# Performance work log

Hardware: AMD Instinct MI355X
Metric: run time of the kernel (lower is better)

## Reference

```python
import jax, jax.numpy as jnp
import numpy as np

# dims
IMG = 24; B = 2; C = 3; N = IMG * IMG + 1        # 577 tokens (patch size 1 + cls)
DIM = 512; DEPTH = 2; H = 8; DH = 64; MLP = 2048; NCLS = 1000
SW = 32      # sliding window size
CB = 16      # compress block size
CS = 4       # compress block sliding stride
SB = 64      # selection block size
KSEL = 4     # num selected blocks


def _ln(x, g, b):
    m = x.mean(-1, keepdims=True)
    v = ((x - m) ** 2).mean(-1, keepdims=True)
    return (x - m) * jax.lax.rsqrt(v + 1e-5) * g + b


# gather rows per (batch, head): t [n, d], i [n, m] -> [n, m, d]
_gather = jax.vmap(jax.vmap(lambda t, i: t[i]))


def _sparse_attn(x, Wq, Wk, Wv, Wg, Wo, kpe, vpe, Wkc, Wvc):
    """Native-sparse-attention (non-causal): compress + top-k block select + sliding window,
    combined with per-head sigmoid gates computed from the input."""
    b, n, _ = x.shape
    split = lambda t: t.reshape(b, n, H, DH).transpose(0, 2, 1, 3)   # [b,h,n,dh]
    q = split(x @ Wq); k = split(x @ Wk); v = split(x @ Wv)
    scale = DH ** -0.5

    # ---- compressed branch: overlapping blocks of size CB, stride CS, MLP-compressed ----
    nc = -(-n // CS)
    pad = (nc - 1) * CS + CB - n
    kp = jnp.pad(k, ((0, 0), (0, 0), (0, pad), (0, 0)))
    vp = jnp.pad(v, ((0, 0), (0, 0), (0, pad), (0, 0)))
    widx = jnp.arange(nc)[:, None] * CS + jnp.arange(CB)[None, :]    # [nc, CB]
    kw = kp[:, :, widx] + kpe                                        # [b,h,nc,CB,dh]
    vw = vp[:, :, widx] + vpe
    ck = kw.reshape(b, H, nc, CB * DH) @ Wkc                         # [b,h,nc,dh]
    cv = vw.reshape(b, H, nc, CB * DH) @ Wvc
    sc = jnp.einsum('bhid,bhjd->bhij', q, ck) * scale                # [b,h,n,nc]
    pc = jax.nn.softmax(sc, axis=-1)
    out_c = jnp.einsum('bhij,bhjd->bhid', pc, cv)

    # ---- selection branch: map compressed-block scores to selection blocks, top-k ----
    ns = -(-n // SB)
    centers = jnp.clip((jnp.arange(nc) * CS + CB // 2) // SB, 0, ns - 1)
    M = jax.nn.one_hot(centers, ns, dtype=pc.dtype)                  # [nc, ns]
    imp = jnp.einsum('bhij,js->bhis', pc, M)                         # [b,h,n,ns]
    _, selb = jax.lax.top_k(imp, KSEL)                               # [b,h,n,KSEL]
    tok = (selb[..., None] * SB + jnp.arange(SB)).reshape(b, H, n, KSEL * SB)
    mask = tok < n
    tokc = jnp.minimum(tok, n - 1)
    kg = _gather(k, tokc)                                            # [b,h,n,KSEL*SB,dh]
    vg = _gather(v, tokc)
    ss = jnp.einsum('bhid,bhikd->bhik', q, kg) * scale
    ss = jnp.where(mask, ss, -jnp.inf)
    ps = jax.nn.softmax(ss, axis=-1)
    out_s = jnp.einsum('bhik,bhikd->bhid', ps, vg)

    # ---- sliding window branch ----
    off = jnp.arange(SW) - SW // 2
    pos = jnp.arange(n)[:, None] + off                               # [n, SW]
    wmask = (pos >= 0) & (pos < n)
    posc = jnp.clip(pos, 0, n - 1)
    kwn = k[:, :, posc]; vwn = v[:, :, posc]                         # [b,h,n,SW,dh]
    sw = jnp.einsum('bhid,bhiwd->bhiw', q, kwn) * scale
    sw = jnp.where(wmask, sw, -jnp.inf)
    pw = jax.nn.softmax(sw, axis=-1)
    out_w = jnp.einsum('bhiw,bhiwd->bhid', pw, vwn)

    # ---- gated combine ----
    g = jax.nn.sigmoid(x @ Wg).reshape(b, n, H, 3).transpose(0, 2, 1, 3)  # [b,h,n,3]
    out = g[..., 0:1] * out_c + g[..., 1:2] * out_s + g[..., 2:3] * out_w
    return out.transpose(0, 2, 1, 3).reshape(b, n, H * DH) @ Wo


def _forward(img, patch_w, patch_b, pos_emb, cls_tok, ln1_g, ln1_b, Wq, Wk, Wv,
             Wg, Wo, kpe, vpe, Wkc, Wvc, ln2_g, ln2_b, ff_w1, ff_b1, ff_w2,
             ff_b2, hln_g, hln_b, head_w, head_b):
    b = img.shape[0]
    # patch size 1: b c h w -> b (h w) c, then linear embed
    x = img.transpose(0, 2, 3, 1).reshape(b, IMG * IMG, C) @ patch_w + patch_b
    x = jnp.concatenate([jnp.broadcast_to(cls_tok, (b, 1, DIM)), x], axis=1)
    x = x + pos_emb[:, :x.shape[1]]
    for l in range(DEPTH):
        h = _ln(x, ln1_g[l], ln1_b[l])
        x = _sparse_attn(h, Wq[l], Wk[l], Wv[l], Wg[l], Wo[l], kpe[l], vpe[l], Wkc[l], Wvc[l]) + x
        h = _ln(x, ln2_g[l], ln2_b[l])
        x = (jax.nn.gelu(h @ ff_w1[l] + ff_b1[l]) @ ff_w2[l] + ff_b2[l]) + x
    x = _ln(x[:, 0], hln_g, hln_b)   # cls pool + head LayerNorm
    return x @ head_w + head_b


def setup_inputs() -> dict:
    key = jax.random.key(0)
    ks = jax.random.split(key, 20)
    rn = lambda k, shape, s=0.02: jax.random.normal(k, shape, dtype=jnp.float32) * s
    d = {}
    d['img'] = jax.random.normal(ks[0], (B, C, IMG, IMG), dtype=jnp.float32)
    d['patch_w'] = rn(ks[1], (C, DIM), 0.2)
    d['patch_b'] = jnp.zeros((DIM,), jnp.float32)
    d['pos_emb'] = rn(ks[2], (1, N, DIM))
    d['cls_tok'] = rn(ks[3], (1, 1, DIM))
    d['ln1_g'] = jnp.ones((DEPTH, DIM), jnp.float32)
    d['ln1_b'] = jnp.zeros((DEPTH, DIM), jnp.float32)
    d['Wq'] = rn(ks[4], (DEPTH, DIM, H * DH))
    d['Wk'] = rn(ks[5], (DEPTH, DIM, H * DH))
    d['Wv'] = rn(ks[6], (DEPTH, DIM, H * DH))
    d['Wg'] = rn(ks[7], (DEPTH, DIM, 3 * H))
    d['Wo'] = rn(ks[8], (DEPTH, H * DH, DIM))
    d['kpe'] = rn(ks[9], (DEPTH, CB, DH))
    d['vpe'] = rn(ks[10], (DEPTH, CB, DH))
    d['Wkc'] = rn(ks[11], (DEPTH, CB * DH, DH))
    d['Wvc'] = rn(ks[12], (DEPTH, CB * DH, DH))
    d['ln2_g'] = jnp.ones((DEPTH, DIM), jnp.float32)
    d['ln2_b'] = jnp.zeros((DEPTH, DIM), jnp.float32)
    d['ff_w1'] = rn(ks[13], (DEPTH, DIM, MLP))
    d['ff_b1'] = jnp.zeros((DEPTH, MLP), jnp.float32)
    d['ff_w2'] = rn(ks[14], (DEPTH, MLP, DIM))
    d['ff_b2'] = jnp.zeros((DEPTH, DIM), jnp.float32)
    d['hln_g'] = jnp.ones((DIM,), jnp.float32)
    d['hln_b'] = jnp.zeros((DIM,), jnp.float32)
    d['head_w'] = rn(ks[15], (DIM, NCLS))
    d['head_b'] = jnp.zeros((NCLS,), jnp.float32)
    return d


def reference(img, patch_w, patch_b, pos_emb, cls_tok, ln1_g, ln1_b, Wq, Wk, Wv,
              Wg, Wo, kpe, vpe, Wkc, Wvc, ln2_g, ln2_b, ff_w1, ff_b1, ff_w2,
              ff_b2, hln_g, hln_b, head_w, head_b):
    return _forward(img, patch_w, patch_b, pos_emb, cls_tok, ln1_g, ln1_b, Wq, Wk, Wv,
                    Wg, Wo, kpe, vpe, Wkc, Wvc, ln2_g, ln2_b, ff_w1, ff_b1, ff_w2,
                    ff_b2, hln_g, hln_b, head_w, head_b)
```

## Files before the change

### kernel.cpp

```cpp
#include <hip/hip_runtime.h>
#include <math.h>


#define NTOK 577
#define DIMD 512
#define NH 8
#define DHD 64
#define NC 145
#define NSB 10
#define KSELD 4
#define SBD 64
#define CBD 16
#define CSD 4
#define SWD 32
#define MLPD 2048
#define NCLSD 1000
#define BATCH 2
#define QKVN 1536
#define QKVNG 1600
#define SFSTRIDE 592
#define SCSTRIDE 160
#define PSTRIDE 832
#define MCKD 2320

typedef unsigned short ushort;
typedef __attribute__((ext_vector_type(8))) short short8;
typedef __attribute__((ext_vector_type(4))) short short4v;
typedef __attribute__((ext_vector_type(4))) float f32x4;

#if defined(__has_builtin)
#if __has_builtin(__builtin_amdgcn_global_load_lds)
#define HAVE_GLL 1
#endif
#endif

#ifdef HAVE_GLL
__device__ __forceinline__ void gll16(const ushort* g, short* l) {
  __builtin_amdgcn_global_load_lds(
      (const __attribute__((address_space(1))) unsigned int*)g,
      (__attribute__((address_space(3))) unsigned int*)l, 16, 0, 0);
}
#endif

__device__ __forceinline__ ushort bf16_rne(float f) {
  union { float f; unsigned u; } v; v.f = f;
  unsigned u = v.u;
  unsigned r = (u + 0x7fffu + ((u >> 16) & 1u)) >> 16;
  return (ushort)r;
}
__device__ __forceinline__ float bf16_to_f(ushort s) {
  union { unsigned u; float f; } v; v.u = ((unsigned)s) << 16;
  return v.f;
}
__device__ __forceinline__ int imin(int a, int b) { return a < b ? a : b; }
__device__ __forceinline__ int imax(int a, int b) { return a > b ? a : b; }

__global__ void prep_kernel(const float* __restrict__ Wq, const float* __restrict__ Wk,
                            const float* __restrict__ Wv, const float* __restrict__ Wg,
                            const float* __restrict__ Wo, const float* __restrict__ Wkc,
                            const float* __restrict__ Wvc, const float* __restrict__ w1,
                            const float* __restrict__ w2,
                            ushort* __restrict__ wqkv_t, ushort* __restrict__ wo_t,
                            ushort* __restrict__ w1_t, ushort* __restrict__ w2_t,
                            ushort* __restrict__ wkc_t, ushort* __restrict__ wvc_t,
                            const float* __restrict__ img, const float* __restrict__ pw,
                            const float* __restrict__ pb, const float* __restrict__ pos,
                            const float* __restrict__ cls, float* __restrict__ x) {
  int bid = blockIdx.x;
  int tid = threadIdx.x;
  if (bid >= 6464) {
    int idx = (bid - 6464) * 256 + tid;
    const int total = BATCH * NTOK * DIMD;
    if (idx >= total) return;
    int d = idx & (DIMD - 1);
    int i = (idx / DIMD) % NTOK;
    int b = idx / (DIMD * NTOK);
    float val;
    if (i == 0) {
      val = cls[d];
    } else {
      int p = i - 1;
      val = pb[d];
#pragma unroll
      for (int c = 0; c < 3; ++c)
        val += img[b * 3 * 576 + c * 576 + p] * pw[c * DIMD + d];
    }
    x[idx] = val + pos[i * DIMD + d];
    return;
  }
  __shared__ float tile[32][33];
  int l = bid / 3232;
  int t = bid % 3232;
  const float* W; ushort* Wt; int K, N, bx, by;
  if (t < 768) {
    int which = t >> 8, rr = t & 255;
    W = (which == 0 ? Wq : (which == 1 ? Wk : Wv)) + (long)l * 512 * 512;
    Wt = wqkv_t + (long)l * QKVNG * 512 + which * 512 * 512;
    K = 512; N = 512; bx = rr & 15; by = rr >> 4;
  } else if (t < 1024) {
    int rr = t - 768; W = Wo + (long)l * 512 * 512; Wt = wo_t + (long)l * 512 * 512;
    K = 512; N = 512; bx = rr & 15; by = rr >> 4;
  } else if (t < 2048) {
    int rr = t - 1024; W = w1 + (long)l * 512 * 2048; Wt = w1_t + (long)l * 2048 * 512;
    K = 512; N = 2048; bx = rr & 63; by = rr >> 6;
  } else if (t < 3072) {
    int rr = t - 2048; W = w2 + (long)l * 2048 * 512; Wt = w2_t + (long)l * 512 * 2048;
    K = 2048; N = 512; bx = rr & 15; by = rr >> 4;
  } else if (t < 3104) {
    int rr = t - 3072; W = Wg + (long)l * 512 * 24;
    Wt = wqkv_t + (long)l * QKVNG * 512 + (long)1536 * 512;
    K = 512; N = 24; bx = rr & 1; by = rr >> 1;
  } else if (t < 3168) {
    int rr = t - 3104; W = Wkc + (long)l * 1024 * 64; Wt = wkc_t + (long)l * 64 * 1024;
    K = 1024; N = 64; bx = rr & 1; by = rr >> 1;
  } else {
    int rr = t - 3168; W = Wvc + (long)l * 1024 * 64; Wt = wvc_t + (long)l * 64 * 1024;
    K = 1024; N = 64; bx = rr & 1; by = rr >> 1;
  }
  int k0 = by * 32, n0 = bx * 32;
  int tx = tid & 31, ty = tid >> 5;
#pragma unroll
  for (int r = 0; r < 32; r += 8)
    tile[ty + r][tx] = (n0 + tx < N) ? W[(long)(k0 + ty + r) * N + n0 + tx] : 0.f;
  __syncthreads();
#pragma unroll
  for (int r = 0; r < 32; r += 8)
    Wt[(long)(n0 + ty + r) * K + k0 + tx] = bf16_rne(tile[tx][ty + r]);
}

__global__ void ln_kernel(const float* __restrict__ x, const float* __restrict__ g,
                          const float* __restrict__ bb, ushort* __restrict__ out_bf) {
  int row = blockIdx.x;
  const float* xr = x + (long)row * DIMD;
  int t = threadIdx.x;
  float a = xr[t], c = xr[t + 256];
  __shared__ float s1[256], s2[256];
  s1[t] = a + c;
  s2[t] = a * a + c * c;
  __syncthreads();
  for (int off = 128; off > 0; off >>= 1) {
    if (t < off) { s1[t] += s1[t + off]; s2[t] += s2[t + off]; }
    __syncthreads();
  }
  float m = s1[0] * (1.0f / 512.0f);
  float var = s2[0] * (1.0f / 512.0f) - m * m;
  float r = rsqrtf(var + 1e-5f);
  out_bf[(long)row * DIMD + t] = bf16_rne((a - m) * r * g[t] + bb[t]);
  out_bf[(long)row * DIMD + t + 256] = bf16_rne((c - m) * r * g[t + 256] + bb[t + 256]);
}

__global__ __launch_bounds__(256) void mfma_gemm(
    const ushort* __restrict__ A, const ushort* __restrict__ Bt,
    const float* __restrict__ bias,
    float* __restrict__ Cf, ushort* __restrict__ Cbf, float* __restrict__ gb,
    int M, int N, int K, int kSlice, int mode) {
  int tid = threadIdx.x;
  int lane = tid & 63, wave = tid >> 6;
  int wm = wave >> 1, wn = wave & 1;
  int rowBase = blockIdx.y * 64, colBase = blockIdx.x * 64;
  int m = lane & 15, kg = lane >> 4;
  int kBeg = blockIdx.z * kSlice;
  int kEnd = imin(K, kBeg + kSlice);
  f32x4 acc[2][2] = {};
#ifdef HAVE_GLL
  __shared__ short As[64 * 64];
  __shared__ short Bs[64 * 64];
  int r8 = lane >> 3;
  int cs = (lane & 7) ^ r8;
  const ushort* aG0 = A + (long)(rowBase + wave * 8 + r8) * K + cs * 8 + kBeg;
  const ushort* aG1 = aG0 + (long)32 * K;
  const ushort* bG0 = Bt + (long)(colBase + wave * 8 + r8) * K + cs * 8 + kBeg;
  const ushort* bG1 = bG0 + (long)32 * K;
  short* lA0 = &As[(wave * 8) * 64];
  short* lA1 = &As[(wave * 8 + 32) * 64];
  short* lB0 = &Bs[(wave * 8) * 64];
  short* lB1 = &Bs[(wave * 8 + 32) * 64];
  int xa = m & 7;
  for (int k0 = 0; k0 < kEnd - kBeg; k0 += 64) {
    gll16(aG0 + k0, lA0);
    gll16(aG1 + k0, lA1);
    gll16(bG0 + k0, lB0);
    gll16(bG1 + k0, lB1);
    __syncthreads();
#pragma unroll
    for (int ks = 0; ks < 2; ++ks) {
      int kc = ks * 4 + kg;
      short8 a0 = *(const short8*)&As[(wm * 32 + m) * 64 + (kc ^ xa) * 8];
      short8 a1 = *(const short8*)&As[(wm * 32 + 16 + m) * 64 + (kc ^ xa) * 8];
      short8 b0 = *(const short8*)&Bs[(wn * 32 + m) * 64 + (kc ^ xa) * 8];
      short8 b1 = *(const short8*)&Bs[(wn * 32 + 16 + m) * 64 + (kc ^ xa) * 8];
      acc[0][0] = __builtin_amdgcn_mfma_f32_16x16x32_bf16(a0, b0, acc[0][0], 0, 0, 0);
      acc[0][1] = __builtin_amdgcn_mfma_f32_16x16x32_bf16(a0, b1, acc[0][1], 0, 0, 0);
      acc[1][0] = __builtin_amdgcn_mfma_f32_16x16x32_bf16(a1, b0, acc[1][0], 0, 0, 0);
      acc[1][1] = __builtin_amdgcn_mfma_f32_16x16x32_bf16(a1, b1, acc[1][1], 0, 0, 0);
    }
    __syncthreads();
  }
#else
  __shared__ short As[64][72];
  __shared__ short Bs[64][72];
  for (int k0 = kBeg; k0 < kEnd; k0 += 64) {
#pragma unroll
    for (int cc = 0; cc < 2; ++cc) {
      int c = tid * 2 + cc;
      int r = c >> 3, kc = c & 7;
      short8 av = {};
      int gr = rowBase + r;
      if (gr < M) av = *(const short8*)(A + (long)gr * K + k0 + kc * 8);
      *(short8*)&As[r][kc * 8] = av;
      short8 bv = *(const short8*)(Bt + (long)(colBase + r) * K + k0 + kc * 8);
      *(short8*)&Bs[r][kc * 8] = bv;
    }
    __syncthreads();
#pragma unroll
    for (int ks = 0; ks < 2; ++ks) {
      short8 a0 = *(const short8*)&As[wm * 32 + m][ks * 32 + kg * 8];
      short8 a1 = *(const short8*)&As[wm * 32 + 16 + m][ks * 32 + kg * 8];
      short8 b0 = *(const short8*)&Bs[wn * 32 + m][ks * 32 + kg * 8];
      short8 b1 = *(const short8*)&Bs[wn * 32 + 16 + m][ks * 32 + kg * 8];
      acc[0][0] = __builtin_amdgcn_mfma_f32_16x16x32_bf16(a0, b0, acc[0][0], 0, 0, 0);
      acc[0][1] = __builtin_amdgcn_mfma_f32_16x16x32_bf16(a0, b1, acc[0][1], 0, 0, 0);
      acc[1][0] = __builtin_amdgcn_mfma_f32_16x16x32_bf16(a1, b0, acc[1][0], 0, 0, 0);
      acc[1][1] = __builtin_amdgcn_mfma_f32_16x16x32_bf16(a1, b1, acc[1][1], 0, 0, 0);
    }
    __syncthreads();
  }
#endif
#pragma unroll
  for (int mt = 0; mt < 2; ++mt)
#pragma unroll
    for (int nt = 0; nt < 2; ++nt) {
      int col = colBase + wn * 32 + nt * 16 + m;
#pragma unroll
      for (int r = 0; r < 4; ++r) {
        int row = rowBase + wm * 32 + mt * 16 + kg * 4 + r;
        if (row >= M) continue;
        float v = acc[mt][nt][r];
        if (mode == 2) {
          if (col < QKVN) Cbf[(long)row * QKVN + col] = bf16_rne(v);
          else if (col < QKVNG) gb[(long)row * 64 + (col - QKVN)] = 1.f / (1.f + __expf(-v));
        } else if (mode == 1) {
          v += bias[col];
          float u = 0.7978845608028654f * (v + 0.044715f * v * v * v);
          v = 0.5f * v * (1.f + tanhf(u));
          Cbf[(long)row * N + col] = bf16_rne(v);
        } else {
          if (bias && blockIdx.z == 0) v += bias[col];
          atomicAdd(&Cf[(long)row * N + col], v);
        }
      }
    }
}

__global__ __launch_bounds__(256) void ckcv_gemm(
    const ushort* __restrict__ kwm, const ushort* __restrict__ vwm,
    const ushort* __restrict__ wkc_t, const ushort* __restrict__ wvc_t,
    ushort* __restrict__ ckb, ushort* __restrict__ Vt) {
  const int K = 1024;
  bool cvpath = blockIdx.z != 0;
  const ushort* A  = cvpath ? wvc_t : kwm;
  const ushort* Bt = cvpath ? vwm : wkc_t;
  int rowBase = cvpath ? 0 : blockIdx.y * 64;
  int colBase = cvpath ? blockIdx.y * 64 : 0;
  int aRows = cvpath ? 64 : MCKD;
  int bRows = cvpath ? MCKD : 64;
  __shared__ short As[64][72];
  __shared__ short Bs[64][72];
  int tid = threadIdx.x;
  int lane = tid & 63, wave = tid >> 6;
  int wm = wave >> 1, wn = wave & 1;
  int m = lane & 15, kg = lane >> 4;
  f32x4 acc[2][2] = {};
  for (int k0 = 0; k0 < K; k0 += 64) {
#pragma unroll
    for (int cc = 0; cc < 2; ++cc) {
      int c = tid * 2 + cc;
      int r = c >> 3, kc = c & 7;
      short8 av = {};
      if (rowBase + r < aRows) av = *(const short8*)(A + (long)(rowBase + r) * K + k0 + kc * 8);
      *(short8*)&As[r][kc * 8] = av;
      short8 bv = {};
      if (colBase + r < bRows) bv = *(const short8*)(Bt + (long)(colBase + r) * K + k0 + kc * 8);
      *(short8*)&Bs[r][kc * 8] = bv;
    }
    __syncthreads();
#pragma unroll
    for (int ks = 0; ks < 2; ++ks) {
      short8 a0 = *(const short8*)&As[wm * 32 + m][ks * 32 + kg * 8];
      short8 a1 = *(const short8*)&As[wm * 32 + 16 + m][ks * 32 + kg * 8];
      short8 b0 = *(const short8*)&Bs[wn * 32 + m][ks * 32 + kg * 8];
      short8 b1 = *(const short8*)&Bs[wn * 32 + 16 + m][ks * 32 + kg * 8];
      acc[0][0] = __builtin_amdgcn_mfma_f32_16x16x32_bf16(a0, b0, acc[0][0], 0, 0, 0);
      acc[0][1] = __builtin_amdgcn_mfma_f32_16x16x32_bf16(a0, b1, acc[0][1], 0, 0, 0);
      acc[1][0] = __builtin_amdgcn_mfma_f32_16x16x32_bf16(a1, b0, acc[1][0], 0, 0, 0);
      acc[1][1] = __builtin_amdgcn_mfma_f32_16x16x32_bf16(a1, b1, acc[1][1], 0, 0, 0);
    }
    __syncthreads();
  }
#pragma unroll
  for (int mt = 0; mt < 2; ++mt)
#pragma unroll
    for (int nt = 0; nt < 2; ++nt) {
      int col = colBase + wn * 32 + nt * 16 + m;
#pragma unroll
      for (int r = 0; r < 4; ++r) {
        int row = rowBase + wm * 32 + mt * 16 + kg * 4 + r;
        float v = acc[mt][nt][r];
        if (!cvpath) {
          if (row < MCKD) ckb[(long)row * DHD + col] = bf16_rne(v);
        } else {
          if (col < MCKD) {
            int z16 = col / NC, j = col - z16 * NC;
            Vt[((long)z16 * 64 + row) * PSTRIDE + 640 + j] = bf16_rne(v);
          }
        }
      }
    }
}

__global__ __launch_bounds__(256) void score_kernel(
    const ushort* __restrict__ qkv_bf, const ushort* __restrict__ ckb,
    ushort* __restrict__ Sf, ushort* __restrict__ Scb, float scale) {
  __shared__ short As[64][72];
  __shared__ short Bs[64][72];
  int z = blockIdx.z;
  int b = z >> 3, h = z & 7;
  int i0 = blockIdx.y * 64;
  int xb = blockIdx.x;
  bool isC = xb >= 10;
  int j0 = (isC ? (xb - 10) : xb) * 64;
  int tid = threadIdx.x;
  int lane = tid & 63, wave = tid >> 6;
  int wm = wave >> 1, wn = wave & 1;
  const ushort* aBase = qkv_bf + (long)b * NTOK * QKVN + h * 64;
  const ushort* bBase = aBase + 512;
  const ushort* cBase = ckb + (long)z * NC * DHD;
#pragma unroll
  for (int rep = 0; rep < 4; ++rep) {
    int row = rep * 16 + (tid >> 4);
    int c4 = tid & 15;
    int gi = i0 + row;
    short4v a16 = {};
    if (gi < NTOK) a16 = *(const short4v*)(aBase + (long)gi * QKVN + c4 * 4);
    *(short4v*)&As[row][c4 * 4] = a16;
    int gj = j0 + row;
    short4v b16 = {};
    if (isC) {
      if (gj < NC) b16 = *(const short4v*)(cBase + (long)gj * DHD + c4 * 4);
    } else {
      if (gj < NTOK) b16 = *(const short4v*)(bBase + (long)gj * QKVN + c4 * 4);
    }
    *(short4v*)&Bs[row][c4 * 4] = b16;
  }
  __syncthreads();
  int m = lane & 15, kg = lane >> 4;
  f32x4 acc[2][2] = {};
#pragma unroll
  for (int ks = 0; ks < 2; ++ks) {
    short8 a0 = *(const short8*)&As[wm * 32 + m][ks * 32 + kg * 8];
    short8 a1 = *(const short8*)&As[wm * 32 + 16 + m][ks * 32 + kg * 8];
    short8 b0 = *(const short8*)&Bs[wn * 32 + m][ks * 32 + kg * 8];
    short8 b1 = *(const short8*)&Bs[wn * 32 + 16 + m][ks * 32 + kg * 8];
    acc[0][0] = __builtin_amdgcn_mfma_f32_16x16x32_bf16(a0, b0, acc[0][0], 0, 0, 0);
    acc[0][1] = __builtin_amdgcn_mfma_f32_16x16x32_bf16(a0, b1, acc[0][1], 0, 0, 0);
    acc[1][0] = __builtin_amdgcn_mfma_f32_16x16x32_bf16(a1, b0, acc[1][0], 0, 0, 0);
    acc[1][1] = __builtin_amdgcn_mfma_f32_16x16x32_bf16(a1, b1, acc[1][1], 0, 0, 0);
  }
  int nvalid = isC ? NC : NTOK;
  int sstride = isC ? SCSTRIDE : SFSTRIDE;
  ushort* Sz = (isC ? Scb : Sf) + (long)z * NTOK * sstride;
#pragma unroll
  for (int mt = 0; mt < 2; ++mt)
#pragma unroll
    for (int nt = 0; nt < 2; ++nt) {
      int col = j0 + wn * 32 + nt * 16 + m;
#pragma unroll
      for (int r = 0; r < 4; ++r) {
        int row = i0 + wm * 32 + mt * 16 + kg * 4 + r;
        if (row < NTOK && col < nvalid)
          Sz[(long)row * sstride + col] = bf16_rne(acc[mt][nt][r] * scale);
      }
    }
}

__global__ void kwvt_kernel(const ushort* __restrict__ qkv_bf,
                            const float* __restrict__ kpe, const float* __restrict__ vpe,
                            ushort* __restrict__ kwm, ushort* __restrict__ vwm,
                            ushort* __restrict__ Vt) {
  __shared__ short tile[64][72];
  int bid = blockIdx.x;
  if (bid < MCKD) {
    int j = bid % NC;
    int bh = bid / NC;
    int h = bh & 7, b = bh >> 3;
    int t = threadIdx.x >> 4;
    int d4 = threadIdx.x & 15;
    int tok = j * CSD + t;
    float k0 = 0.f, k1 = 0.f, k2 = 0.f, k3 = 0.f, v0 = 0.f, v1 = 0.f, v2 = 0.f, v3 = 0.f;
    if (tok < NTOK) {
      const ushort* base = qkv_bf + (long)(b * NTOK + tok) * QKVN + h * DHD + d4 * 4;
      short4v kv = *(const short4v*)(base + 512);
      short4v vv = *(const short4v*)(base + 1024);
      k0 = bf16_to_f((ushort)kv.x); k1 = bf16_to_f((ushort)kv.y);
      k2 = bf16_to_f((ushort)kv.z); k3 = bf16_to_f((ushort)kv.w);
      v0 = bf16_to_f((ushort)vv.x); v1 = bf16_to_f((ushort)vv.y);
      v2 = bf16_to_f((ushort)vv.z); v3 = bf16_to_f((ushort)vv.w);
    }
    float4 kp = *(const float4*)(kpe + t * DHD + d4 * 4);
    float4 vp = *(const float4*)(vpe + t * DHD + d4 * 4);
    short4v ko, vo;
    ko.x = (short)bf16_rne(k0 + kp.x); ko.y = (short)bf16_rne(k1 + kp.y);
    ko.z = (short)bf16_rne(k2 + kp.z); ko.w = (short)bf16_rne(k3 + kp.w);
    vo.x = (short)bf16_rne(v0 + vp.x); vo.y = (short)bf16_rne(v1 + vp.y);
    vo.z = (short)bf16_rne(v2 + vp.z); vo.w = (short)bf16_rne(v3 + vp.w);
    long ob = (long)bid * 1024 + t * DHD + d4 * 4;
    *(short4v*)(kwm + ob) = ko;
    *(short4v*)(vwm + ob) = vo;
  } else {
    int t = bid - MCKD;
    int kt = t % 10, z = t / 10;
    int b = z >> 3, h = z & 7;
    int tid = threadIdx.x;
    int r = tid >> 2, seg = tid & 3;
    short8 a0 = {}, a1 = {};
    int tok = kt * 64 + r;
    if (tok < NTOK) {
      const ushort* src = qkv_bf + (long)(b * NTOK + tok) * QKVN + 1024 + h * 64 + seg * 16;
      a0 = *(const short8*)src;
      a1 = *(const short8*)(src + 8);
    }
    *(short8*)&tile[r][seg * 16] = a0;
    *(short8*)&tile[r][seg * 16 + 8] = a1;
    __syncthreads();
    int d = tid >> 2;
    short8 o0, o1;
#pragma unroll
    for (int q = 0; q < 8; ++q) o0[q] = tile[seg * 16 + q][d];
#pragma unroll
    for (int q = 0; q < 8; ++q) o1[q] = tile[seg * 16 + 8 + q][d];
    ushort* dst = Vt + ((long)z * 64 + d) * PSTRIDE + kt * 64 + seg * 16;
    *(short8*)dst = o0;
    *(short8*)(dst + 8) = o1;
  }
}

__global__ __launch_bounds__(256, 4) void prob_kernel(
    const ushort* __restrict__ Sf, const ushort* __restrict__ Scb,
    const float* __restrict__ gb, ushort* __restrict__ P) {
  int qt = blockIdx.x % NC;
  int z = blockIdx.x / NC;
  int h = z & 7, b = z >> 3;
  int tid = threadIdx.x, lane = tid & 63, w = tid >> 6;
  int i0 = qt * 4 + w;
  bool valid = i0 < NTOK;
  int i = imin(i0, NTOK - 1);

  __shared__ float scL[4][192];
  __shared__ float ssL[4][256];
  __shared__ float swL[4][32];
  __shared__ float impL[4][16];
  __shared__ int selL[4][KSELD];
  float* sc = scL[w]; float* ss = ssL[w];
  float* swv = swL[w]; float* imp = impL[w]; int* sel = selL[w];

  const ushort* scRow = Scb + ((long)z * NTOK + i) * SCSTRIDE;
  const ushort* sfRow = Sf + ((long)z * NTOK + i) * SFSTRIDE;

  float e[3], mC = -1e30f;
#pragma unroll
  for (int c = 0; c < 3; ++c) {
    int j = c * 64 + lane;
    float s = bf16_to_f(scRow[imin(j, NC - 1)]);
    s = (j < NC) ? s : -1e30f;
    e[c] = s;
    mC = fmaxf(mC, s);
  }
#pragma unroll
  for (int msk = 1; msk < 64; msk <<= 1) mC = fmaxf(mC, __shfl_xor(mC, msk, 64));
  float sumC = 0.f;
#pragma unroll
  for (int c = 0; c < 3; ++c) {
    float ev = (e[c] > -1e29f) ? __expf(e[c] - mC) : 0.f;
    sc[c * 64 + lane] = ev;
    sumC += ev;
  }
#pragma unroll
  for (int msk = 1; msk < 64; msk <<= 1) sumC += __shfl_xor(sumC, msk, 64);
  __syncthreads();

  if (lane < NSB) {
    int lo = imax(0, 16 * lane - 2), hi = imin(NC - 1, 16 * lane + 13);
    float s = 0.f;
    for (int j = lo; j <= hi; ++j) s += sc[j];
    imp[lane] = s;
  }
  __syncthreads();
  if (lane == 0) {
    unsigned used = 0;
    for (int r = 0; r < KSELD; ++r) {
      int bi = 0; float bv = -1e30f;
      for (int s = 0; s < NSB; ++s)
        if (!((used >> s) & 1u) && imp[s] > bv) { bv = imp[s]; bi = s; }
      used |= 1u << bi;
      sel[r] = bi;
    }
  }
  __syncthreads();

  float es[4], mS = -1e30f;
#pragma unroll
  for (int c = 0; c < 4; ++c) {
    int tok = sel[c] * SBD + lane;
    float s = bf16_to_f(sfRow[imin(tok, NTOK - 1)]);
    s = (tok < NTOK) ? s : -1e30f;
    es[c] = s;
    mS = fmaxf(mS, s);
  }
#pragma unroll
  for (int msk = 1; msk < 64; msk <<= 1) mS = fmaxf(mS, __shfl_xor(mS, msk, 64));
  float sumS = 0.f;
#pragma unroll
  for (int c = 0; c < 4; ++c) {
    float ev = (es[c] > -1e29f) ? __expf(es[c] - mS) : 0.f;
    ss[c * 64 + lane] = ev;
    sumS += ev;
  }
#pragma unroll
  for (int msk = 1; msk < 64; msk <<= 1) sumS += __shfl_xor(sumS, msk, 64);

  float sw_s;
  {
    int pos = i + (lane & 31) - SWD / 2;
    float s = bf16_to_f(sfRow[imin(imax(pos, 0), NTOK - 1)]);
    sw_s = (pos >= 0 && pos < NTOK) ? s : -1e30f;
  }
  float mW = sw_s;
#pragma unroll
  for (int msk = 1; msk < 32; msk <<= 1) mW = fmaxf(mW, __shfl_xor(mW, msk, 64));
  float ew = (sw_s > -1e29f) ? __expf(sw_s - mW) : 0.f;
  float sumW = ew;
#pragma unroll
  for (int msk = 1; msk < 32; msk <<= 1) sumW += __shfl_xor(sumW, msk, 64);
  if (lane < SWD) swv[lane] = ew;
  __syncthreads();

  if (!valid) return;
  const float* gp = gb + (long)(b * NTOK + i) * 64 + h * 3;
  float rC = gp[0] / sumC, rS = gp[1] / sumS, rW = gp[2] / sumW;
  ushort* prow = P + ((long)z * NTOK + i0) * PSTRIDE;
#pragma unroll
  for (int c = 0; c < 10; ++c) {
    int col = c * 64 + lane;
    float val = 0.f;
#pragma unroll
    for (int r = 0; r < 4; ++r)
      if (sel[r] == c) val += rS * ss[r * 64 + lane];
    int t = col - i + 16;
    if (t >= 0 && t < SWD && col < NTOK) val += rW * swv[t];
    prow[col] = bf16_rne(val);
  }
#pragma unroll
  for (int c = 0; c < 3; ++c) {
    int j = c * 64 + lane;
    float val = (j < NC) ? rC * sc[j] : 0.f;
    prow[640 + j] = bf16_rne(val);
  }
}

__global__ __launch_bounds__(256) void pv_gemm(const ushort* __restrict__ P,
                                               const ushort* __restrict__ Vt,
                                               ushort* __restrict__ comb) {
  __shared__ short As[64][72];
  __shared__ short Bs[64][72];
  int z = blockIdx.y;
  int b = z >> 3, h = z & 7;
  int rowBase = blockIdx.x * 64;
  int tid = threadIdx.x;
  int lane = tid & 63, wave = tid >> 6;
  int wm = wave >> 1, wn = wave & 1;
  const ushort* Pz = P + (long)z * NTOK * PSTRIDE;
  const ushort* Vz = Vt + (long)z * 64 * PSTRIDE;
  int m = lane & 15, kg = lane >> 4;
  f32x4 acc[2][2] = {};
  for (int k0 = 0; k0 < PSTRIDE; k0 += 64) {
#pragma unroll
    for (int cc = 0; cc < 2; ++cc) {
      int c = tid * 2 + cc;
      int r = c >> 3, kc = c & 7;
      short8 av = {};
      int gr = rowBase + r;
      if (gr < NTOK) av = *(const short8*)(Pz + (long)gr * PSTRIDE + k0 + kc * 8);
      *(short8*)&As[r][kc * 8] = av;
      short8 bv = *(const short8*)(Vz + (long)r * PSTRIDE + k0 + kc * 8);
      *(short8*)&Bs[r][kc * 8] = bv;
    }
    __syncthreads();
#pragma unroll
    for (int ks = 0; ks < 2; ++ks) {
      short8 a0 = *(const short8*)&As[wm * 32 + m][ks * 32 + kg * 8];
      short8 a1 = *(const short8*)&As[wm * 32 + 16 + m][ks * 32 + kg * 8];
      short8 b0 = *(const short8*)&Bs[wn * 32 + m][ks * 32 + kg * 8];
      short8 b1 = *(const short8*)&Bs[wn * 32 + 16 + m][ks * 32 + kg * 8];
      acc[0][0] = __builtin_amdgcn_mfma_f32_16x16x32_bf16(a0, b0, acc[0][0], 0, 0, 0);
      acc[0][1] = __builtin_amdgcn_mfma_f32_16x16x32_bf16(a0, b1, acc[0][1], 0, 0, 0);
      acc[1][0] = __builtin_amdgcn_mfma_f32_16x16x32_bf16(a1, b0, acc[1][0], 0, 0, 0);
      acc[1][1] = __builtin_amdgcn_mfma_f32_16x16x32_bf16(a1, b1, acc[1][1], 0, 0, 0);
    }
    __syncthreads();
  }
#pragma unroll
  for (int mt = 0; mt < 2; ++mt)
#pragma unroll
    for (int nt = 0; nt < 2; ++nt) {
      int col = wn * 32 + nt * 16 + m;
#pragma unroll
      for (int r = 0; r < 4; ++r) {
        int row = rowBase + wm * 32 + mt * 16 + kg * 4 + r;
        if (row < NTOK)
          comb[(long)(b * NTOK + row) * DIMD + h * 64 + col] = bf16_rne(acc[mt][nt][r]);
      }
    }
}

__global__ void head_kernel(const float* __restrict__ x, const float* __restrict__ hg,
                            const float* __restrict__ hb, const float* __restrict__ W,
                            const float* __restrict__ bias, float* __restrict__ out) {
  int b = blockIdx.y;
  int tid = threadIdx.x;
  const float* xr = x + (long)b * NTOK * DIMD;
  __shared__ float red1[256], red2[256];
  float a = xr[tid], c = xr[tid + 256];
  red1[tid] = a + c;
  red2[tid] = a * a + c * c;
  __syncthreads();
  for (int off = 128; off > 0; off >>= 1) {
    if (tid < off) { red1[tid] += red1[tid + off]; red2[tid] += red2[tid + off]; }
    __syncthreads();
  }
  float m = red1[0] * (1.f / 512.f);
  float var = red2[0] * (1.f / 512.f) - m * m;
  float rs = rsqrtf(var + 1e-5f);
  __shared__ float hs[512];
  hs[tid] = (a - m) * rs * hg[tid] + hb[tid];
  hs[tid + 256] = (c - m) * rs * hg[tid + 256] + hb[tid + 256];
  __syncthreads();
  int col = blockIdx.x * 64 + (tid & 63);
  int ks = tid >> 6;
  float acc = 0.f;
  if (col < NCLSD) {
    for (int k = ks * 128; k < ks * 128 + 128; ++k)
      acc += hs[k] * W[(long)k * NCLSD + col];
  }
  __shared__ float part[4][64];
  part[ks][tid & 63] = acc;
  __syncthreads();
  if (tid < 64) {
    int c2 = blockIdx.x * 64 + tid;
    if (c2 < NCLSD)
      out[b * NCLSD + c2] = part[0][tid] + part[1][tid] + part[2][tid] + part[3][tid] + bias[c2];
  }
}

extern "C" void kernel_launch(void* const* d_in, const int* in_sizes, int n_in,
                              void* d_out, int out_size, void* d_ws, size_t ws_size,
                              hipStream_t stream) {
  const float* img     = (const float*)d_in[0];
  const float* patch_w = (const float*)d_in[1];
  const float* patch_b = (const float*)d_in[2];
  const float* pos_emb = (const float*)d_in[3];
  const float* cls_tok = (const float*)d_in[4];
  const float* ln1_g   = (const float*)d_in[5];
  const float* ln1_b   = (const float*)d_in[6];
  const float* Wq      = (const float*)d_in[7];
  const float* Wk      = (const float*)d_in[8];
  const float* Wv      = (const float*)d_in[9];
  const float* Wg      = (const float*)d_in[10];
  const float* Wo      = (const float*)d_in[11];
  const float* kpe     = (const float*)d_in[12];
  const float* vpe     = (const float*)d_in[13];
  const float* Wkc     = (const float*)d_in[14];
  const float* Wvc     = (const float*)d_in[15];
  const float* ln2_g   = (const float*)d_in[16];
  const float* ln2_b   = (const float*)d_in[17];
  const float* ff_w1   = (const float*)d_in[18];
  const float* ff_b1   = (const float*)d_in[19];
  const float* ff_w2   = (const float*)d_in[20];
  const float* ff_b2   = (const float*)d_in[21];
  const float* hln_g   = (const float*)d_in[22];
  const float* hln_b   = (const float*)d_in[23];
  const float* head_w  = (const float*)d_in[24];
  const float* head_b  = (const float*)d_in[25];
  float* out = (float*)d_out;

  char* p = (char*)d_ws;
  const long MROW = (long)BATCH * NTOK;
  float* x       = (float*)p;  p += MROW * DIMD * 4;
  ushort* qkv_bf = (ushort*)p; p += MROW * QKVN * 2;
  ushort* h_bf   = (ushort*)p; p += MROW * DIMD * 2;
  ushort* comb_bf= (ushort*)p; p += MROW * DIMD * 2;
  float* gb      = (float*)p;  p += MROW * 64 * 4;
  ushort* ckb    = (ushort*)p; p += (long)MCKD * DHD * 2;
  ushort* Vt     = (ushort*)p; p += (long)BATCH * NH * 64 * PSTRIDE * 2;
  ushort* Scb    = (ushort*)p; p += (long)BATCH * NH * NTOK * SCSTRIDE * 2;
  ushort* wqkv_t = (ushort*)p; p += 2L * QKVNG * DIMD * 2;
  ushort* wo_t   = (ushort*)p; p += 2L * DIMD * DIMD * 2;
  ushort* w1_t   = (ushort*)p; p += 2L * MLPD * DIMD * 2;
  ushort* w2_t   = (ushort*)p; p += 2L * DIMD * MLPD * 2;
  ushort* wkc_t  = (ushort*)p; p += 2L * 64 * 1024 * 2;
  ushort* wvc_t  = (ushort*)p; p += 2L * 64 * 1024 * 2;
  ushort* kwm    = (ushort*)p;
  ushort* vwm    = kwm + (long)MCKD * 1024;
  ushort* P      = kwm;
  p += (long)BATCH * NH * NTOK * PSTRIDE * 2;
  ushort* Sf     = (ushort*)p;
  ushort* ff1_bf = Sf;
  p += (long)BATCH * NH * NTOK * SFSTRIDE * 2;
  p += 64 * 2048 * 2;

  const int M = (int)MROW;
  const int MB64 = (M + 63) / 64;
  const float scale = 0.125f;

  prep_kernel<<<6464 + (int)((M * DIMD + 255) / 256), 256, 0, stream>>>(
      Wq, Wk, Wv, Wg, Wo, Wkc, Wvc, ff_w1, ff_w2,
      wqkv_t, wo_t, w1_t, w2_t, wkc_t, wvc_t,
      img, patch_w, patch_b, pos_emb, cls_tok, x);

  for (int l = 0; l < 2; ++l) {
    const ushort* wqkv_l = wqkv_t + (long)l * QKVNG * DIMD;
    const ushort* wo_l   = wo_t + (long)l * DIMD * DIMD;
    const ushort* w1t_l  = w1_t + (long)l * MLPD * DIMD;
    const ushort* w2t_l  = w2_t + (long)l * DIMD * MLPD;
    const ushort* wkc_l  = wkc_t + (long)l * 64 * 1024;
    const ushort* wvc_l  = wvc_t + (long)l * 64 * 1024;
    const float* kpe_l = kpe + (long)l * CBD * DHD;
    const float* vpe_l = vpe + (long)l * CBD * DHD;
    const float* b1_l  = ff_b1 + (long)l * MLPD;
    const float* b2_l  = ff_b2 + (long)l * DIMD;

    ln_kernel<<<M, 256, 0, stream>>>(x, ln1_g + (long)l * DIMD, ln1_b + (long)l * DIMD, h_bf);
    mfma_gemm<<<dim3(QKVNG / 64, MB64), 256, 0, stream>>>(h_bf, wqkv_l, nullptr, nullptr, qkv_bf, gb, M, QKVNG, DIMD, DIMD, 2);
    kwvt_kernel<<<MCKD + 160, 256, 0, stream>>>(qkv_bf, kpe_l, vpe_l, kwm, vwm, Vt);
    ckcv_gemm<<<dim3(1, (MCKD + 63) / 64, 2), 256, 0, stream>>>(kwm, vwm, wkc_l, wvc_l, ckb, Vt);
    score_kernel<<<dim3(13, 10, BATCH * NH), 256, 0, stream>>>(qkv_bf, ckb, Sf, Scb, scale);
    prob_kernel<<<BATCH * NH * NC, 256, 0, stream>>>(Sf, Scb, gb, P);
    pv_gemm<<<dim3(10, BATCH * NH), 256, 0, stream>>>(P, Vt, comb_bf);
    mfma_gemm<<<dim3(DIMD / 64, MB64, 2), 256, 0, stream>>>(comb_bf, wo_l, nullptr, x, nullptr, nullptr, M, DIMD, DIMD, 256, 4);
    ln_kernel<<<M, 256, 0, stream>>>(x, ln2_g + (long)l * DIMD, ln2_b + (long)l * DIMD, h_bf);
    mfma_gemm<<<dim3(MLPD / 64, MB64), 256, 0, stream>>>(h_bf, w1t_l, b1_l, nullptr, ff1_bf, nullptr, M, MLPD, DIMD, DIMD, 1);
    mfma_gemm<<<dim3(DIMD / 64, MB64, 4), 256, 0, stream>>>(ff1_bf, w2t_l, b2_l, x, nullptr, nullptr, M, DIMD, MLPD, 512, 4);
  }

  head_kernel<<<dim3(16, BATCH), 256, 0, stream>>>(x, hln_g, hln_b, head_w, head_b, out);
}
```

Baseline: 364.7 us.

## Fuse compressed-window gather into ckcv GEMM and V transpose into score kernel

Removes the kwvt_kernel launch. The ckcv GEMM now gathers the overlapping K/V windows straight from qkv_bf and adds the positional embeddings while loading its tiles, so the kwm/vwm intermediates are no longer written and read back. The V transpose into Vt moves into an extra x-slice of the score kernel grid. LayerNorm and head reductions now use wave shuffles instead of shared-memory tree reductions. In exchange, the GEMM loads become scattered and recompute the bf16 add for each tile.

```diff
diff --git a/kernel.cpp b/kernel.cpp
--- a/kernel.cpp
+++ b/kernel.cpp
@@ -54,6 +54,34 @@
 }
 __device__ __forceinline__ int imin(int a, int b) { return a < b ? a : b; }
 __device__ __forceinline__ int imax(int a, int b) { return a > b ? a : b; }
+
+__device__ __forceinline__ short8 gather_pe(const ushort* __restrict__ qkv_bf,
+                                            const float* __restrict__ pe,
+                                            int rIdx, int t, int d, int koff) {
+  int j = rIdx % NC;
+  int bh = rIdx / NC;
+  int h = bh & 7, b = bh >> 3;
+  int tok = j * CSD + t;
+  float v[8];
+  if (tok < NTOK) {
+    const ushort* base = qkv_bf + (long)(b * NTOK + tok) * QKVN + koff + h * DHD + d;
+    short8 raw = *(const short8*)base;
+#pragma unroll
+    for (int q = 0; q < 8; ++q) v[q] = bf16_to_f((ushort)raw[q]);
+  } else {
+#pragma unroll
+    for (int q = 0; q < 8; ++q) v[q] = 0.f;
+  }
+  const float* pp = pe + t * DHD + d;
+  float4 p0 = *(const float4*)pp;
+  float4 p1 = *(const float4*)(pp + 4);
+  short8 o;
+  o[0] = (short)bf16_rne(v[0] + p0.x); o[1] = (short)bf16_rne(v[1] + p0.y);
+  o[2] = (short)bf16_rne(v[2] + p0.z); o[3] = (short)bf16_rne(v[3] + p0.w);
+  o[4] = (short)bf16_rne(v[4] + p1.x); o[5] = (short)bf16_rne(v[5] + p1.y);
+  o[6] = (short)bf16_rne(v[6] + p1.z); o[7] = (short)bf16_rne(v[7] + p1.w);
+  return o;
+}
 
 __global__ void prep_kernel(const float* __restrict__ Wq, const float* __restrict__ Wk,
                             const float* __restrict__ Wv, const float* __restrict__ Wg,
@@ -134,16 +162,21 @@
   const float* xr = x + (long)row * DIMD;
   int t = threadIdx.x;
   float a = xr[t], c = xr[t + 256];
-  __shared__ float s1[256], s2[256];
-  s1[t] = a + c;
-  s2[t] = a * a + c * c;
-  __syncthreads();
-  for (int off = 128; off > 0; off >>= 1) {
-    if (t < off) { s1[t] += s1[t + off]; s2[t] += s2[t + off]; }
-    __syncthreads();
-  }
-  float m = s1[0] * (1.0f / 512.0f);
-  float var = s2[0] * (1.0f / 512.0f) - m * m;
+  float s1 = a + c;
+  float s2 = a * a + c * c;
+#pragma unroll
+  for (int msk = 1; msk < 64; msk <<= 1) {
+    s1 += __shfl_xor(s1, msk, 64);
+    s2 += __shfl_xor(s2, msk, 64);
+  }
+  __shared__ float w1[4], w2[4];
+  int w = t >> 6;
+  if ((t & 63) == 0) { w1[w] = s1; w2[w] = s2; }
+  __syncthreads();
+  float S1 = w1[0] + w1[1] + w1[2] + w1[3];
+  float S2 = w2[0] + w2[1] + w2[2] + w2[3];
+  float m = S1 * (1.0f / 512.0f);
+  float var = S2 * (1.0f / 512.0f) - m * m;
   float r = rsqrtf(var + 1e-5f);
   out_bf[(long)row * DIMD + t] = bf16_rne((a - m) * r * g[t] + bb[t]);
   out_bf[(long)row * DIMD + t + 256] = bf16_rne((c - m) * r * g[t + 256] + bb[t + 256]);
@@ -253,17 +286,14 @@
 }
 
 __global__ __launch_bounds__(256) void ckcv_gemm(
-    const ushort* __restrict__ kwm, const ushort* __restrict__ vwm,
+    const ushort* __restrict__ qkv_bf,
+    const float* __restrict__ kpe, const float* __restrict__ vpe,
     const ushort* __restrict__ wkc_t, const ushort* __restrict__ wvc_t,
     ushort* __restrict__ ckb, ushort* __restrict__ Vt) {
   const int K = 1024;
   bool cvpath = blockIdx.z != 0;
-  const ushort* A  = cvpath ? wvc_t : kwm;
-  const ushort* Bt = cvpath ? vwm : wkc_t;
   int rowBase = cvpath ? 0 : blockIdx.y * 64;
   int colBase = cvpath ? blockIdx.y * 64 : 0;
-  int aRows = cvpath ? 64 : MCKD;
-  int bRows = cvpath ? MCKD : 64;
   __shared__ short As[64][72];
   __shared__ short Bs[64][72];
   int tid = threadIdx.x;
@@ -272,15 +302,23 @@
   int m = lane & 15, kg = lane >> 4;
   f32x4 acc[2][2] = {};
   for (int k0 = 0; k0 < K; k0 += 64) {
+    int t = k0 >> 6;
 #pragma unroll
     for (int cc = 0; cc < 2; ++cc) {
       int c = tid * 2 + cc;
       int r = c >> 3, kc = c & 7;
-      short8 av = {};
-      if (rowBase + r < aRows) av = *(const short8*)(A + (long)(rowBase + r) * K + k0 + kc * 8);
+      int d = kc * 8;
+      short8 av = {}, bv = {};
+      if (!cvpath) {
+        int rIdx = rowBase + r;
+        if (rIdx < MCKD) av = gather_pe(qkv_bf, kpe, rIdx, t, d, 512);
+        bv = *(const short8*)(wkc_t + (long)r * K + k0 + d);
+      } else {
+        av = *(const short8*)(wvc_t + (long)r * K + k0 + d);
+        int cIdx = colBase + r;
+        if (cIdx < MCKD) bv = gather_pe(qkv_bf, vpe, cIdx, t, d, 1024);
+      }
       *(short8*)&As[r][kc * 8] = av;
-      short8 bv = {};
-      if (colBase + r < bRows) bv = *(const short8*)(Bt + (long)(colBase + r) * K + k0 + kc * 8);
       *(short8*)&Bs[r][kc * 8] = bv;
     }
     __syncthreads();
@@ -320,16 +358,41 @@
 
 __global__ __launch_bounds__(256) void score_kernel(
     const ushort* __restrict__ qkv_bf, const ushort* __restrict__ ckb,
-    ushort* __restrict__ Sf, ushort* __restrict__ Scb, float scale) {
+    ushort* __restrict__ Sf, ushort* __restrict__ Scb, ushort* __restrict__ Vt,
+    float scale) {
   __shared__ short As[64][72];
   __shared__ short Bs[64][72];
   int z = blockIdx.z;
   int b = z >> 3, h = z & 7;
+  int xb = blockIdx.x;
+  int tid = threadIdx.x;
+  if (xb == 13) {
+    int kt = blockIdx.y;
+    int r = tid >> 2, seg = tid & 3;
+    short8 a0 = {}, a1 = {};
+    int tok = kt * 64 + r;
+    if (tok < NTOK) {
+      const ushort* src = qkv_bf + (long)(b * NTOK + tok) * QKVN + 1024 + h * 64 + seg * 16;
+      a0 = *(const short8*)src;
+      a1 = *(const short8*)(src + 8);
+    }
+    *(short8*)&As[r][seg * 16] = a0;
+    *(short8*)&As[r][seg * 16 + 8] = a1;
+    __syncthreads();
+    int d = tid >> 2;
+    short8 o0, o1;
+#pragma unroll
+    for (int q = 0; q < 8; ++q) o0[q] = As[seg * 16 + q][d];
+#pragma unroll
+    for (int q = 0; q < 8; ++q) o1[q] = As[seg * 16 + 8 + q][d];
+    ushort* dst = Vt + ((long)z * 64 + d) * PSTRIDE + kt * 64 + seg * 16;
+    *(short8*)dst = o0;
+    *(short8*)(dst + 8) = o1;
+    return;
+  }
   int i0 = blockIdx.y * 64;
-  int xb = blockIdx.x;
   bool isC = xb >= 10;
   int j0 = (isC ? (xb - 10) : xb) * 64;
-  int tid = threadIdx.x;
   int lane = tid & 63, wave = tid >> 6;
   int wm = wave >> 1, wn = wave & 1;
   const ushort* aBase = qkv_bf + (long)b * NTOK * QKVN + h * 64;
@@ -381,67 +444,6 @@
           Sz[(long)row * sstride + col] = bf16_rne(acc[mt][nt][r] * scale);
       }
     }
-}
-
-__global__ void kwvt_kernel(const ushort* __restrict__ qkv_bf,
-                            const float* __restrict__ kpe, const float* __restrict__ vpe,
-                            ushort* __restrict__ kwm, ushort* __restrict__ vwm,
-                            ushort* __restrict__ Vt) {
-  __shared__ short tile[64][72];
-  int bid = blockIdx.x;
-  if (bid < MCKD) {
-    int j = bid % NC;
-    int bh = bid / NC;
-    int h = bh & 7, b = bh >> 3;
-    int t = threadIdx.x >> 4;
-    int d4 = threadIdx.x & 15;
-    int tok = j * CSD + t;
-    float k0 = 0.f, k1 = 0.f, k2 = 0.f, k3 = 0.f, v0 = 0.f, v1 = 0.f, v2 = 0.f, v3 = 0.f;
-    if (tok < NTOK) {
-      const ushort* base = qkv_bf + (long)(b * NTOK + tok) * QKVN + h * DHD + d4 * 4;
-      short4v kv = *(const short4v*)(base + 512);
-      short4v vv = *(const short4v*)(base + 1024);
-      k0 = bf16_to_f((ushort)kv.x); k1 = bf16_to_f((ushort)kv.y);
-      k2 = bf16_to_f((ushort)kv.z); k3 = bf16_to_f((ushort)kv.w);
-      v0 = bf16_to_f((ushort)vv.x); v1 = bf16_to_f((ushort)vv.y);
-      v2 = bf16_to_f((ushort)vv.z); v3 = bf16_to_f((ushort)vv.w);
-    }
-    float4 kp = *(const float4*)(kpe + t * DHD + d4 * 4);
-    float4 vp = *(const float4*)(vpe + t * DHD + d4 * 4);
-    short4v ko, vo;
-    ko.x = (short)bf16_rne(k0 + kp.x); ko.y = (short)bf16_rne(k1 + kp.y);
-    ko.z = (short)bf16_rne(k2 + kp.z); ko.w = (short)bf16_rne(k3 + kp.w);
-    vo.x = (short)bf16_rne(v0 + vp.x); vo.y = (short)bf16_rne(v1 + vp.y);
-    vo.z = (short)bf16_rne(v2 + vp.z); vo.w = (short)bf16_rne(v3 + vp.w);
-    long ob = (long)bid * 1024 + t * DHD + d4 * 4;
-    *(short4v*)(kwm + ob) = ko;
-    *(short4v*)(vwm + ob) = vo;
-  } else {
-    int t = bid - MCKD;
-    int kt = t % 10, z = t / 10;
-    int b = z >> 3, h = z & 7;
-    int tid = threadIdx.x;
-    int r = tid >> 2, seg = tid & 3;
-    short8 a0 = {}, a1 = {};
-    int tok = kt * 64 + r;
-    if (tok < NTOK) {
-      const ushort* src = qkv_bf + (long)(b * NTOK + tok) * QKVN + 1024 + h * 64 + seg * 16;
-      a0 = *(const short8*)src;
-      a1 = *(const short8*)(src + 8);
-    }
-    *(short8*)&tile[r][seg * 16] = a0;
-    *(short8*)&tile[r][seg * 16 + 8] = a1;
-    __syncthreads();
-    int d = tid >> 2;
-    short8 o0, o1;
-#pragma unroll
-    for (int q = 0; q < 8; ++q) o0[q] = tile[seg * 16 + q][d];
-#pragma unroll
-    for (int q = 0; q < 8; ++q) o1[q] = tile[seg * 16 + 8 + q][d];
-    ushort* dst = Vt + ((long)z * 64 + d) * PSTRIDE + kt * 64 + seg * 16;
-    *(short8*)dst = o0;
-    *(short8*)(dst + 8) = o1;
-  }
 }
 
 __global__ __launch_bounds__(256, 4) void prob_kernel(
@@ -628,17 +630,20 @@
   int b = blockIdx.y;
   int tid = threadIdx.x;
   const float* xr = x + (long)b * NTOK * DIMD;
-  __shared__ float red1[256], red2[256];
   float a = xr[tid], c = xr[tid + 256];
-  red1[tid] = a + c;
-  red2[tid] = a * a + c * c;
-  __syncthreads();
-  for (int off = 128; off > 0; off >>= 1) {
-    if (tid < off) { red1[tid] += red1[tid + off]; red2[tid] += red2[tid + off]; }
-    __syncthreads();
-  }
-  float m = red1[0] * (1.f / 512.f);
-  float var = red2[0] * (1.f / 512.f) - m * m;
+  float s1 = a + c, s2 = a * a + c * c;
+#pragma unroll
+  for (int msk = 1; msk < 64; msk <<= 1) {
+    s1 += __shfl_xor(s1, msk, 64);
+    s2 += __shfl_xor(s2, msk, 64);
+  }
+  __shared__ float w1[4], w2[4];
+  if ((tid & 63) == 0) { w1[tid >> 6] = s1; w2[tid >> 6] = s2; }
+  __syncthreads();
+  float S1 = w1[0] + w1[1] + w1[2] + w1[3];
+  float S2 = w2[0] + w2[1] + w2[2] + w2[3];
+  float m = S1 * (1.f / 512.f);
+  float var = S2 * (1.f / 512.f) - m * m;
   float rs = rsqrtf(var + 1e-5f);
   __shared__ float hs[512];
   hs[tid] = (a - m) * rs * hg[tid] + hb[tid];
@@ -708,10 +713,7 @@
   ushort* w2_t   = (ushort*)p; p += 2L * DIMD * MLPD * 2;
   ushort* wkc_t  = (ushort*)p; p += 2L * 64 * 1024 * 2;
   ushort* wvc_t  = (ushort*)p; p += 2L * 64 * 1024 * 2;
-  ushort* kwm    = (ushort*)p;
-  ushort* vwm    = kwm + (long)MCKD * 1024;
-  ushort* P      = kwm;
-  p += (long)BATCH * NH * NTOK * PSTRIDE * 2;
+  ushort* P      = (ushort*)p; p += (long)BATCH * NH * NTOK * PSTRIDE * 2;
   ushort* Sf     = (ushort*)p;
   ushort* ff1_bf = Sf;
   p += (long)BATCH * NH * NTOK * SFSTRIDE * 2;
@@ -740,9 +742,8 @@
 
     ln_kernel<<<M, 256, 0, stream>>>(x, ln1_g + (long)l * DIMD, ln1_b + (long)l * DIMD, h_bf);
     mfma_gemm<<<dim3(QKVNG / 64, MB64), 256, 0, stream>>>(h_bf, wqkv_l, nullptr, nullptr, qkv_bf, gb, M, QKVNG, DIMD, DIMD, 2);
-    kwvt_kernel<<<MCKD + 160, 256, 0, stream>>>(qkv_bf, kpe_l, vpe_l, kwm, vwm, Vt);
-    ckcv_gemm<<<dim3(1, (MCKD + 63) / 64, 2), 256, 0, stream>>>(kwm, vwm, wkc_l, wvc_l, ckb, Vt);
-    score_kernel<<<dim3(13, 10, BATCH * NH), 256, 0, stream>>>(qkv_bf, ckb, Sf, Scb, scale);
+    ckcv_gemm<<<dim3(1, (MCKD + 63) / 64, 2), 256, 0, stream>>>(qkv_bf, kpe_l, vpe_l, wkc_l, wvc_l, ckb, Vt);
+    score_kernel<<<dim3(14, 10, BATCH * NH), 256, 0, stream>>>(qkv_bf, ckb, Sf, Scb, Vt, scale);
     prob_kernel<<<BATCH * NH * NC, 256, 0, stream>>>(Sf, Scb, gb, P);
     pv_gemm<<<dim3(10, BATCH * NH), 256, 0, stream>>>(P, Vt, comb_bf);
     mfma_gemm<<<dim3(DIMD / 64, MB64, 2), 256, 0, stream>>>(comb_bf, wo_l, nullptr, x, nullptr, nullptr, M, DIMD, DIMD, 256, 4);
```

Measured after the change: 368.8 us. No clear change (+1.1%).
